# Kernel optimization log

Hardware: AMD Instinct MI355X
Metric: run time of the kernel (lower is better)

The kernel has to match this reference:

```python
import jax, jax.numpy as jnp
import numpy as np

RADIUS = 0.2
NSAMPLE = 32
GROUPS = 4
EPS = 1e-5


def group_norm(x, gamma, beta):
    # x: [B, C, *spatial]; normalize per (batch, group) over channels-in-group + spatial
    B, C = x.shape[0], x.shape[1]
    rest = x.shape[2:]
    xr = x.reshape(B, GROUPS, -1)
    mean = xr.mean(-1, keepdims=True)
    var = xr.var(-1, keepdims=True)
    xr = (xr - mean) * jax.lax.rsqrt(var + EPS)
    x = xr.reshape((B, C) + rest)
    bshape = (1, C) + (1,) * len(rest)
    return x * gamma.reshape(bshape) + beta.reshape(bshape)


def ball_query(pos_t):
    # pos_t: [B, N, 3] -> idx [B, N, NSAMPLE] (query points == all points)
    N = pos_t.shape[1]
    sq = jnp.sum(pos_t * pos_t, axis=-1)  # [B, N]
    d = sq[:, :, None] + sq[:, None, :] - 2.0 * jnp.einsum('bnc,bmc->bnm', pos_t, pos_t)
    ar = jnp.arange(N, dtype=jnp.int32)
    gi = jnp.where(d > RADIUS * RADIUS, N, ar[None, None, :])  # [B, S, N]
    gi = jnp.sort(gi, axis=-1)[:, :, :NSAMPLE]  # ascending in-ball indices first
    first = gi[:, :, :1]
    gi = jnp.where(gi == N, first, gi)  # pad with first neighbor
    return gi


def setup_inputs() -> dict:
    key = jax.random.key(0)
    ks = jax.random.split(key, 6)
    B, C, N = 2, 64, 4096
    M = 4 * C  # mid channels
    return {
        'x': jax.random.normal(ks[0], (B, C, N), jnp.float32),
        'pos': jax.random.uniform(ks[1], (B, 3, N), jnp.float32),
        'w1': jax.random.normal(ks[2], (M, C), jnp.float32) * 0.05,
        'b1': jnp.zeros((M,), jnp.float32),
        'g1': jnp.ones((M,), jnp.float32),
        'be1': jnp.zeros((M,), jnp.float32),
        'wd': 1.0 + jax.random.normal(ks[3], (M,), jnp.float32) * 0.05,
        'gd': jnp.ones((M,), jnp.float32),
        'bed': jnp.zeros((M,), jnp.float32),
        'w2': jax.random.normal(ks[4], (C, M), jnp.float32) * 0.05,
        'b2': jnp.zeros((C,), jnp.float32),
        'g2': jnp.ones((C,), jnp.float32),
        'be2': jnp.zeros((C,), jnp.float32),
    }


def reference(x, pos, w1, b1, g1, be1, wd, gd, bed, w2, b2, g2, be2):
    # x: [B, C, N], pos: [B, 3, N]
    pos_t = jnp.transpose(pos, (0, 2, 1))  # [B, N, 3]
    idx = ball_query(pos_t)  # [B, N, K]

    # conv1 (1x1) -> GroupNorm -> GELU
    h = jnp.einsum('mc,bcn->bmn', w1, x) + b1[None, :, None]
    h = jax.nn.gelu(group_norm(h, g1, be1), approximate=False)  # [B, M, N]

    # gather neighbors: feats [B, N, M] indexed by idx [B, N, K]
    feats = jnp.transpose(h, (0, 2, 1))
    grouped = jax.vmap(lambda f, i: f[i])(feats, idx)  # [B, N, K, M]
    grouped = jnp.transpose(grouped, (0, 3, 1, 2))  # [B, M, N, K]

    # depthwise 1x1 conv (per-channel scale, no bias) -> GroupNorm -> max-pool over K -> GELU
    grouped = grouped * wd[None, :, None, None]
    grouped = group_norm(grouped, gd, bed)
    h2 = jax.nn.gelu(jnp.max(grouped, axis=-1), approximate=False)  # [B, M, N]

    # conv2 (1x1) -> GroupNorm -> residual
    out = jnp.einsum('cm,bmn->bcn', w2, h2) + b2[None, :, None]
    out = group_norm(out, g2, be2)
    return out + x
```

## Files before the change

kernel.cpp:

```cpp
#include <hip/hip_runtime.h>
#include <hip/hip_fp16.h>
#include <math.h>

#define BB 2
#define CC 64
#define NN 4096
#define MM 256
#define KK 32
#define GG 4
#define EPSF 1e-5f

__device__ __forceinline__ float gelu_exact(float x) {
    return 0.5f * x * (1.0f + erff(x * 0.70710678118654752f));
}

__device__ __forceinline__ unsigned pkmax(unsigned a, unsigned b) {
    unsigned d;
    asm volatile("v_pk_max_f16 %0, %1, %2" : "=v"(d) : "v"(a), "v"(b));
    return d;
}
__device__ __forceinline__ unsigned pkmin(unsigned a, unsigned b) {
    unsigned d;
    asm volatile("v_pk_min_f16 %0, %1, %2" : "=v"(d) : "v"(a), "v"(b));
    return d;
// ... 59 lines not shown
        o[1][2] = fmaf(wv.y, xv.z, o[1][2]); o[1][3] = fmaf(wv.y, xv.w, o[1][3]);
        o[2][0] = fmaf(wv.z, xv.x, o[2][0]); o[2][1] = fmaf(wv.z, xv.y, o[2][1]);
        o[2][2] = fmaf(wv.z, xv.z, o[2][2]); o[2][3] = fmaf(wv.z, xv.w, o[2][3]);
        o[3][0] = fmaf(wv.w, xv.x, o[3][0]); o[3][1] = fmaf(wv.w, xv.y, o[3][1]);
        o[3][2] = fmaf(wv.w, xv.z, o[3][2]); o[3][3] = fmaf(wv.w, xv.w, o[3][3]);
    }

    float s1 = 0.f, s2 = 0.f;
    #pragma unroll
    for (int mi = 0; mi < 4; mi++) {
        int m = m0 + mseg * 4 + mi;
        float bv = b1[m];
        float4 r;
        r.x = o[mi][0] + bv; r.y = o[mi][1] + bv;
        r.z = o[mi][2] + bv; r.w = o[mi][3] + bv;
        *(float4*)&h[((size_t)(b * MM + m)) * NN + n0 + nq * 4] = r;
        s1 += r.x + r.y + r.z + r.w;
        s2 = fmaf(r.x, r.x, s2); s2 = fmaf(r.y, r.y, s2);
        s2 = fmaf(r.z, r.z, s2); s2 = fmaf(r.w, r.w, s2);
    }
    for (int off = 32; off; off >>= 1) {
        s1 += __shfl_down(s1, off, 64);
        s2 += __shfl_down(s2, off, 64);
    }
    int w = t >> 6, l = t & 63;
    if (l == 0) { r1[w] = s1; r2[w] = s2; }
    __syncthreads();
    if (t == 0) {
        Mp[bx] = make_float2(r1[0] + r1[1] + r1[2] + r1[3],
                             r2[0] + r2[1] + r2[2] + r2[3]);
    }
}

__global__ void k_gn1t(const float* __restrict__ h, const float* __restrict__ g1,
                       const float* __restrict__ be1, const float* __restrict__ wd,
                       const float2* __restrict__ Mp, __half* __restrict__ pH,
                       float* __restrict__ R) {
    __shared__ float tile[64 * 65];
    __shared__ float mv[2];
    int n0 = blockIdx.x * 64;
    int m0 = blockIdx.y * 64;
    int b  = blockIdx.z;
    int g  = blockIdx.y;
    int t = threadIdx.x;

    if (t < 64) {
        float2 p2 = Mp[b * 256 + g * 64 + t];
        float s1 = p2.x, s2 = p2.y;
        for (int off = 32; off; off >>= 1) {
            s1 += __shfl_down(s1, off, 64);
            s2 += __shfl_down(s2, off, 64);
        }
        if (t == 0) {
            const double cnt = 64.0 * 4096.0;
            double md = (double)s1 / cnt;
            double vd = (double)s2 / cnt - md * md;
            mv[0] = (float)md;
            mv[1] = rsqrtf((float)vd + EPSF);
        }
    }
    __syncthreads();
    float mean = mv[0], rstd = mv[1];

    int nq = t & 15, mr = t >> 4;
    #pragma unroll
    for (int pp = 0; pp < 4; pp++) {
        int row = pp * 16 + mr;
        int m = m0 + row;
        float a = rstd * g1[m];
        float cc2 = be1[m] - mean * a;
        float wdm = wd[m];
        float4 hv = *(const float4*)&h[((size_t)(b * MM + m)) * NN + n0 + nq * 4];
        tile[row * 65 + nq * 4 + 0] = gelu_exact(fmaf(hv.x, a, cc2)) * wdm;
        tile[row * 65 + nq * 4 + 1] = gelu_exact(fmaf(hv.y, a, cc2)) * wdm;
        tile[row * 65 + nq * 4 + 2] = gelu_exact(fmaf(hv.z, a, cc2)) * wdm;
        tile[row * 65 + nq * 4 + 3] = gelu_exact(fmaf(hv.w, a, cc2)) * wdm;
    }
    __syncthreads();
    #pragma unroll
    for (int pp = 0; pp < 4; pp++) {
        int id = pp * 256 + t;
        int nl = id >> 4, mq = id & 15;
        float a0 = tile[(mq * 4 + 0) * 65 + nl];
        float a1 = tile[(mq * 4 + 1) * 65 + nl];
        float a2 = tile[(mq * 4 + 2) * 65 + nl];
        float a3 = tile[(mq * 4 + 3) * 65 + nl];
        __half2 hA = __float22half2_rn(make_float2(a0, a1));
        __half2 hB = __float22half2_rn(make_float2(a2, a3));
        uint2 st8;
        st8.x = *(unsigned*)&hA; st8.y = *(unsigned*)&hB;
        *(uint2*)((char*)pH + ((((size_t)(b * NN) + n0 + nl)) << 9) + (m0 + mq * 4) * 2) = st8;
        float2 fa = __half22float2(hA);
        float2 fb = __half22float2(hB);
        float t1 = fa.x + fa.y + fb.x + fb.y;
        float t2 = fa.x * fa.x + fa.y * fa.y + fb.x * fb.x + fb.y * fb.y;
        #pragma unroll
        for (int off = 8; off; off >>= 1) {
            t1 += __shfl_down(t1, off, 16);
            t2 += __shfl_down(t2, off, 16);
        }
        if ((t & 15) == 0) {
            float* rr = &R[((size_t)(b * NN) + n0 + nl) * 8];
            rr[g]     = t1;
            rr[4 + g] = t2;
        }
    }
}

__global__ void k_ballq(const float* __restrict__ pos, int* __restrict__ idx) {
    int wid  = blockIdx.x * 4 + (threadIdx.x >> 6);
    int lane = threadIdx.x & 63;
    int b = wid >> 12;
    int n = wid & 4095;
    const float* px = pos + b * 3 * NN;
    const float* py = px + NN;
    const float* pz = py + NN;
    float qx = px[n], qy = py[n], qz = pz[n];
    float qsq = qx*qx + qy*qy + qz*qz;
    int* row = idx + (b * NN + n) * KK;

    int found = 0;
    int first = -1;
    const float R2 = 0.04f;
    for (int m0 = 0; m0 < NN && found < KK; m0 += 64) {
        int m = m0 + lane;
        float ax = px[m], ay = py[m], az = pz[m];
        float msq = ax*ax + ay*ay + az*az;
        float dot = qx*ax + qy*ay + qz*az;
        float d = qsq + msq - 2.0f * dot;
        bool hit = !(d > R2);
        unsigned long long mask = __ballot(hit);
        if (first < 0 && mask) first = m0 + (__ffsll((long long)mask) - 1);
        unsigned long long lt = (lane == 0) ? 0ULL : (mask & ((1ULL << lane) - 1ULL));
        int posh = __popcll(lt);
        if (hit && (found + posh) < KK) row[found + posh] = m;
        found += __popcll(mask);
        if (found > KK) found = KK;
    }
    if (lane < KK && lane >= found) row[lane] = first;
}

__global__ __launch_bounds__(256)
void k_qgather(const __half* __restrict__ pH, const int* __restrict__ idx,
               const float* __restrict__ R, const float* __restrict__ gd,
               __half* __restrict__ pselH, float* __restrict__ Rp) {
    int t = threadIdx.x, w = t >> 6, l = t & 63;
    int gn = blockIdx.x * 4 + w;
    int b = gn >> 12;

    int hh = l >> 5, cl = l & 31;
    int myidx = idx[gn * KK + cl];
    const char* pb = (const char*)(pH + (size_t)b * NN * 256);
    int laneoff = cl * 16;

    unsigned vmax0 = 0xFC00FC00u, vmax1 = 0xFC00FC00u, vmax2 = 0xFC00FC00u, vmax3 = 0xFC00FC00u;
    unsigned vmin0 = 0x7C007C00u, vmin1 = 0x7C007C00u, vmin2 = 0x7C007C00u, vmin3 = 0x7C007C00u;

    #pragma unroll
    for (int k = 0; k < 16; k++) {
        int ja = __shfl(myidx, 2 * k, 64);
        int jb = __shfl(myidx, 2 * k + 1, 64);
        int j = hh ? jb : ja;
        uint4 raw = *(const uint4*)(pb + (((size_t)j) << 9) + laneoff);
        vmax0 = pkmax(vmax0, raw.x); vmin0 = pkmin(vmin0, raw.x);
        vmax1 = pkmax(vmax1, raw.y); vmin1 = pkmin(vmin1, raw.y);
        vmax2 = pkmax(vmax2, raw.z); vmin2 = pkmin(vmin2, raw.z);
        vmax3 = pkmax(vmax3, raw.w); vmin3 = pkmin(vmin3, raw.w);
    }
    vmax0 = pkmax(vmax0, (unsigned)__shfl_xor((int)vmax0, 32, 64));
    vmax1 = pkmax(vmax1, (unsigned)__shfl_xor((int)vmax1, 32, 64));
    vmax2 = pkmax(vmax2, (unsigned)__shfl_xor((int)vmax2, 32, 64));
    vmax3 = pkmax(vmax3, (unsigned)__shfl_xor((int)vmax3, 32, 64));
    vmin0 = pkmin(vmin0, (unsigned)__shfl_xor((int)vmin0, 32, 64));
    vmin1 = pkmin(vmin1, (unsigned)__shfl_xor((int)vmin1, 32, 64));
    vmin2 = pkmin(vmin2, (unsigned)__shfl_xor((int)vmin2, 32, 64));
    vmin3 = pkmin(vmin3, (unsigned)__shfl_xor((int)vmin3, 32, 64));

    if (hh == 0) {
        const float4* g4 = (const float4*)gd;
        float4 gA = g4[cl * 2], gB = g4[cl * 2 + 1];
        uint4 out;
        out.x = selpair(vmax0, vmin0, gA.x, gA.y);
        out.y = selpair(vmax1, vmin1, gA.z, gA.w);
        out.z = selpair(vmax2, vmin2, gB.x, gB.y);
        out.w = selpair(vmax3, vmin3, gB.z, gB.w);
        *(uint4*)((char*)pselH + (((size_t)gn) << 9) + laneoff) = out;
    } else {
        const float* rr = &R[((size_t)(b * NN) + myidx) * 8];
        float4 ra = *(const float4*)rr;
        float4 rb = *(const float4*)(rr + 4);
        float s[8] = {ra.x, ra.y, ra.z, ra.w, rb.x, rb.y, rb.z, rb.w};
        #pragma unroll
        for (int off = 16; off; off >>= 1) {
            #pragma unroll
            for (int c = 0; c < 8; c++) s[c] += __shfl_down(s[c], off, 32);
        }
        if (cl == 0) {
            float4* rp = (float4*)&Rp[(size_t)gn * 8];
            rp[0] = make_float4(s[0], s[1], s[2], s[3]);
            rp[1] = make_float4(s[4], s[5], s[6], s[7]);
        }
    }
}

__global__ __launch_bounds__(256, 4)
void k_mlp2(const __half* __restrict__ pselH, const float* __restrict__ Rp,
            const float* __restrict__ w2, const float* __restrict__ b2,
            const float* __restrict__ gd, const float* __restrict__ bed,
            float* __restrict__ oraw, float* __restrict__ Op) {
    __shared__ float w2s[64 * 257];
    __shared__ float sw[4][8];
    __shared__ float sA[4][4], sB[4][4];

    int t = threadIdx.x;
    int w = t >> 6, l = t & 63;
    int b  = blockIdx.x >> 8;
    int n0 = (blockIdx.x & 255) * 16 + w * 4;

    #pragma unroll
    for (int p = 0; p < 16; p++) {
        int i = p * 256 + t;
        int c = i >> 6, mq = i & 63;
        float4 v = ((const float4*)w2)[i];
        float* dst = &w2s[c * 257 + mq * 4];
        dst[0] = v.x; dst[1] = v.y; dst[2] = v.z; dst[3] = v.w;
    }

    {
        const float4* rp = (const float4*)(Rp + (size_t)b * NN * 8);
        float s[8] = {0.f, 0.f, 0.f, 0.f, 0.f, 0.f, 0.f, 0.f};
        #pragma unroll
        for (int r = 0; r < 16; r++) {
            float4 ra = rp[(t * 16 + r) * 2];
            float4 rb = rp[(t * 16 + r) * 2 + 1];
            s[0] += ra.x; s[1] += ra.y; s[2] += ra.z; s[3] += ra.w;
            s[4] += rb.x; s[5] += rb.y; s[6] += rb.z; s[7] += rb.w;
        }
        #pragma unroll
        for (int off = 32; off; off >>= 1) {
            #pragma unroll
            for (int c = 0; c < 8; c++) s[c] += __shfl_down(s[c], off, 64);
        }
        if (l == 0) {
            #pragma unroll
            for (int c = 0; c < 8; c++) sw[w][c] = s[c];
        }
    }
    __syncthreads();

    int g = l >> 4;
    double s1 = (double)sw[0][g] + sw[1][g] + sw[2][g] + sw[3][g];
    double s2 = (double)sw[0][4 + g] + sw[1][4 + g] + sw[2][4 + g] + sw[3][4 + g];
    const double cnt2 = 64.0 * 4096.0 * 32.0;
    double m_ = s1 / cnt2;
    double v_ = s2 / cnt2 - m_ * m_;
    float mean = (float)m_;
    float rstd = rsqrtf((float)v_ + EPSF);
    float4 gd4  = ((const float4*)gd)[l];
    float4 bed4 = ((const float4*)bed)[l];
    float ax = rstd * gd4.x, ay = rstd * gd4.y, az = rstd * gd4.z, aw = rstd * gd4.w;
    float cx = bed4.x - mean * ax, cy = bed4.y - mean * ay;
    float cz = bed4.z - mean * az, cw = bed4.w - mean * aw;

    float4 h2r[4];
    #pragma unroll
    for (int j = 0; j < 4; j++) {
        uint2 raw = *(const uint2*)((const char*)pselH +
                     ((((size_t)(b * NN)) + n0 + j) << 9) + l * 8);
        float2 fa = __half22float2(*(__half2*)&raw.x);
        float2 fb = __half22float2(*(__half2*)&raw.y);
        h2r[j].x = gelu_exact(fmaf(fa.x, ax, cx));
        h2r[j].y = gelu_exact(fmaf(fa.y, ay, cy));
        h2r[j].z = gelu_exact(fmaf(fb.x, az, cz));
        h2r[j].w = gelu_exact(fmaf(fb.y, aw, cw));
    }

    const float* w2l = &w2s[l * 257];
    float acc[4] = {0.f, 0.f, 0.f, 0.f};
    #pragma unroll 8
    for (int mq = 0; mq < 64; mq++) {
        float w0  = w2l[4 * mq + 0];
        float w1_ = w2l[4 * mq + 1];
        float w2_ = w2l[4 * mq + 2];
        float w3_ = w2l[4 * mq + 3];
        #pragma unroll
        for (int j = 0; j < 4; j++) {
            acc[j] = fmaf(w0,  bcast_lane(h2r[j].x, mq), acc[j]);
            acc[j] = fmaf(w1_, bcast_lane(h2r[j].y, mq), acc[j]);
            acc[j] = fmaf(w2_, bcast_lane(h2r[j].z, mq), acc[j]);
            acc[j] = fmaf(w3_, bcast_lane(h2r[j].w, mq), acc[j]);
        }
    }

    float bias = b2[l];
    float so1 = 0.f, so2 = 0.f;
    #pragma unroll
    for (int j = 0; j < 4; j++) {
        acc[j] += bias;
        so1 += acc[j];
        so2 = fmaf(acc[j], acc[j], so2);
    }
    *(float4*)&oraw[((size_t)(b * CC) + l) * NN + n0] =
        make_float4(acc[0], acc[1], acc[2], acc[3]);

    so1 += __shfl_down(so1, 8, 16); so2 += __shfl_down(so2, 8, 16);
    so1 += __shfl_down(so1, 4, 16); so2 += __shfl_down(so2, 4, 16);
    so1 += __shfl_down(so1, 2, 16); so2 += __shfl_down(so2, 2, 16);
    so1 += __shfl_down(so1, 1, 16); so2 += __shfl_down(so2, 1, 16);
    if ((l & 15) == 0) { sA[w][l >> 4] = so1; sB[w][l >> 4] = so2; }
    __syncthreads();
    if (t < 8) {
        int is2 = t >> 2, gg = t & 3;
        float v = is2 ? (sB[0][gg] + sB[1][gg] + sB[2][gg] + sB[3][gg])
                      : (sA[0][gg] + sA[1][gg] + sA[2][gg] + sA[3][gg]);
        Op[blockIdx.x * 8 + t] = v;
    }
}

__global__ void k_final(const float* __restrict__ oraw, const float* __restrict__ x,
                        const float* __restrict__ g2, const float* __restrict__ be2,
                        const float* __restrict__ Op, float* __restrict__ out) {
    __shared__ float fw[4][8];
    int t = threadIdx.x;
    int i4 = blockIdx.x * 256 + t;
    int base = i4 * 4;
    int b = base >> 18;

    {
        const float4* rp = (const float4*)(Op + ((size_t)b * 256 + t) * 8);
        float4 ra = rp[0], rb = rp[1];
        float s[8] = {ra.x, ra.y, ra.z, ra.w, rb.x, rb.y, rb.z, rb.w};
        #pragma unroll
        for (int off = 32; off; off >>= 1) {
            #pragma unroll
            for (int c = 0; c < 8; c++) s[c] += __shfl_down(s[c], off, 64);
        }
        if ((t & 63) == 0) {
            #pragma unroll
            for (int c = 0; c < 8; c++) fw[t >> 6][c] = s[c];
        }
    }
    __syncthreads();

    int c = (base >> 12) & 63;
    int g = c >> 4;
    double s1 = (double)fw[0][g] + fw[1][g] + fw[2][g] + fw[3][g];
    double s2 = (double)fw[0][4 + g] + fw[1][4 + g] + fw[2][4 + g] + fw[3][4 + g];
    const double cnt = 16.0 * 4096.0;
    double mean_d = s1 / cnt;
    double var_d  = s2 / cnt - mean_d * mean_d;
    float mean = (float)mean_d;
    float rstd = rsqrtf((float)var_d + EPSF);
    float sc = rstd * g2[c];
    float ad = be2[c] - mean * sc;
    float4 o = ((const float4*)oraw)[i4];
    float4 xv = ((const float4*)x)[i4];
    float4 r;
    r.x = fmaf(o.x, sc, ad) + xv.x;
    r.y = fmaf(o.y, sc, ad) + xv.y;
    r.z = fmaf(o.z, sc, ad) + xv.z;
    r.w = fmaf(o.w, sc, ad) + xv.w;
    ((float4*)out)[i4] = r;
}

extern "C" void kernel_launch(void* const* d_in, const int* in_sizes, int n_in,
                              void* d_out, int out_size, void* d_ws, size_t ws_size,
                              hipStream_t stream) {
    const float* x   = (const float*)d_in[0];
    const float* pos = (const float*)d_in[1];
    const float* w1  = (const float*)d_in[2];
    const float* b1  = (const float*)d_in[3];
    const float* g1  = (const float*)d_in[4];
    const float* be1 = (const float*)d_in[5];
    const float* wd  = (const float*)d_in[6];
    const float* gd  = (const float*)d_in[7];
    const float* bed = (const float*)d_in[8];
    const float* w2  = (const float*)d_in[9];
    const float* b2  = (const float*)d_in[10];
    const float* g2  = (const float*)d_in[11];
    const float* be2 = (const float*)d_in[12];
    float* out = (float*)d_out;

    char* wsb = (char*)d_ws;
    float*  h     = (float*)wsb;
    __half* pH    = (__half*)(wsb + 8388608);
    __half* pselH = (__half*)(wsb + 12582912);
    float*  oraw  = (float*)(wsb + 16777216);
    int*    idx   = (int*)(wsb + 18874368);
    float*  R     = (float*)(wsb + 19922944);
    float*  Rp    = (float*)(wsb + 20185088);
    float2* Mp    = (float2*)(wsb + 20447232);
    float*  Op    = (float*)(wsb + 20451328);

    k_mlp1<<<512, 256, 0, stream>>>(x, w1, b1, h, Mp);
    k_gn1t<<<dim3(64, 4, 2), 256, 0, stream>>>(h, g1, be1, wd, Mp, pH, R);
    k_ballq<<<2048, 256, 0, stream>>>(pos, idx);
    k_qgather<<<2048, 256, 0, stream>>>(pH, idx, R, gd, pselH, Rp);
    k_mlp2<<<512, 256, 0, stream>>>(pselH, Rp, w2, b2, gd, bed, oraw, Op);
    k_final<<<512, 256, 0, stream>>>(oraw, x, g2, be2, Op, out);
}
```

Baseline: 155.7 us.

## Fuse GN1 with ball query and fold neighbor gather into second MLP

Merges the GroupNorm1/transpose kernel and the ball-query kernel into one launch, with the block index choosing the role. The neighbor gather and max/min pooling move into the second MLP kernel, so the intermediate pooled-feature buffer is no longer written and re-read. A small new kernel computes the grouped GroupNorm statistics from the per-point partial sums. The second MLP kernel now does 32 random gathers per point with 8-byte loads, and its occupancy hint is lowered from 4 to 2 blocks per CU.

Measured after the change: 166.6 us. +7.0%, slower.

```diff
diff --git a/kernel.cpp b/kernel.cpp
--- a/kernel.cpp
+++ b/kernel.cpp
@@ -115,182 +115,162 @@
     }
 }
 
-__global__ void k_gn1t(const float* __restrict__ h, const float* __restrict__ g1,
-                       const float* __restrict__ be1, const float* __restrict__ wd,
-                       const float2* __restrict__ Mp, __half* __restrict__ pH,
-                       float* __restrict__ R) {
+__global__ void k_gn1t_ballq(const float* __restrict__ h, const float* __restrict__ g1,
+                             const float* __restrict__ be1, const float* __restrict__ wd,
+                             const float2* __restrict__ Mp, __half* __restrict__ pH,
+                             float* __restrict__ R,
+                             const float* __restrict__ pos, int* __restrict__ idx) {
     __shared__ float tile[64 * 65];
     __shared__ float mv[2];
-    int n0 = blockIdx.x * 64;
-    int m0 = blockIdx.y * 64;
-    int b  = blockIdx.z;
-    int g  = blockIdx.y;
     int t = threadIdx.x;
 
-    if (t < 64) {
-        float2 p2 = Mp[b * 256 + g * 64 + t];
-        float s1 = p2.x, s2 = p2.y;
-        for (int off = 32; off; off >>= 1) {
-            s1 += __shfl_down(s1, off, 64);
-            s2 += __shfl_down(s2, off, 64);
-        }
-        if (t == 0) {
-            const double cnt = 64.0 * 4096.0;
-            double md = (double)s1 / cnt;
-            double vd = (double)s2 / cnt - md * md;
-            mv[0] = (float)md;
-            mv[1] = rsqrtf((float)vd + EPSF);
-        }
-    }
-    __syncthreads();
-    float mean = mv[0], rstd = mv[1];
-
-    int nq = t & 15, mr = t >> 4;
-    #pragma unroll
-    for (int pp = 0; pp < 4; pp++) {
-        int row = pp * 16 + mr;
-        int m = m0 + row;
-        float a = rstd * g1[m];
-        float cc2 = be1[m] - mean * a;
-        float wdm = wd[m];
-        float4 hv = *(const float4*)&h[((size_t)(b * MM + m)) * NN + n0 + nq * 4];
-        tile[row * 65 + nq * 4 + 0] = gelu_exact(fmaf(hv.x, a, cc2)) * wdm;
-        tile[row * 65 + nq * 4 + 1] = gelu_exact(fmaf(hv.y, a, cc2)) * wdm;
-        tile[row * 65 + nq * 4 + 2] = gelu_exact(fmaf(hv.z, a, cc2)) * wdm;
-        tile[row * 65 + nq * 4 + 3] = gelu_exact(fmaf(hv.w, a, cc2)) * wdm;
-    }
-    __syncthreads();
-    #pragma unroll
-    for (int pp = 0; pp < 4; pp++) {
-        int id = pp * 256 + t;
-        int nl = id >> 4, mq = id & 15;
-        float a0 = tile[(mq * 4 + 0) * 65 + nl];
-        float a1 = tile[(mq * 4 + 1) * 65 + nl];
-        float a2 = tile[(mq * 4 + 2) * 65 + nl];
-        float a3 = tile[(mq * 4 + 3) * 65 + nl];
-        __half2 hA = __float22half2_rn(make_float2(a0, a1));
-        __half2 hB = __float22half2_rn(make_float2(a2, a3));
-        uint2 st8;
-        st8.x = *(unsigned*)&hA; st8.y = *(unsigned*)&hB;
-        *(uint2*)((char*)pH + ((((size_t)(b * NN) + n0 + nl)) << 9) + (m0 + mq * 4) * 2) = st8;
-        float2 fa = __half22float2(hA);
-        float2 fb = __half22float2(hB);
-        float t1 = fa.x + fa.y + fb.x + fb.y;
-        float t2 = fa.x * fa.x + fa.y * fa.y + fb.x * fb.x + fb.y * fb.y;
-        #pragma unroll
-        for (int off = 8; off; off >>= 1) {
-            t1 += __shfl_down(t1, off, 16);
-            t2 += __shfl_down(t2, off, 16);
-        }
-        if ((t & 15) == 0) {
-            float* rr = &R[((size_t)(b * NN) + n0 + nl) * 8];
-            rr[g]     = t1;
-            rr[4 + g] = t2;
-        }
-    }
-}
-
-__global__ void k_ballq(const float* __restrict__ pos, int* __restrict__ idx) {
-    int wid  = blockIdx.x * 4 + (threadIdx.x >> 6);
-    int lane = threadIdx.x & 63;
-    int b = wid >> 12;
-    int n = wid & 4095;
-    const float* px = pos + b * 3 * NN;
-    const float* py = px + NN;
-    const float* pz = py + NN;
-    float qx = px[n], qy = py[n], qz = pz[n];
-    float qsq = qx*qx + qy*qy + qz*qz;
-    int* row = idx + (b * NN + n) * KK;
-
-    int found = 0;
-    int first = -1;
-    const float R2 = 0.04f;
-    for (int m0 = 0; m0 < NN && found < KK; m0 += 64) {
-        int m = m0 + lane;
-        float ax = px[m], ay = py[m], az = pz[m];
-        float msq = ax*ax + ay*ay + az*az;
-        float dot = qx*ax + qy*ay + qz*az;
-        float d = qsq + msq - 2.0f * dot;
-        bool hit = !(d > R2);
-        unsigned long long mask = __ballot(hit);
-        if (first < 0 && mask) first = m0 + (__ffsll((long long)mask) - 1);
-        unsigned long long lt = (lane == 0) ? 0ULL : (mask & ((1ULL << lane) - 1ULL));
-        int posh = __popcll(lt);
-        if (hit && (found + posh) < KK) row[found + posh] = m;
-        found += __popcll(mask);
-        if (found > KK) found = KK;
-    }
-    if (lane < KK && lane >= found) row[lane] = first;
-}
-
-__global__ __launch_bounds__(256)
-void k_qgather(const __half* __restrict__ pH, const int* __restrict__ idx,
-               const float* __restrict__ R, const float* __restrict__ gd,
-               __half* __restrict__ pselH, float* __restrict__ Rp) {
-    int t = threadIdx.x, w = t >> 6, l = t & 63;
-    int gn = blockIdx.x * 4 + w;
-    int b = gn >> 12;
-
-    int hh = l >> 5, cl = l & 31;
-    int myidx = idx[gn * KK + cl];
-    const char* pb = (const char*)(pH + (size_t)b * NN * 256);
-    int laneoff = cl * 16;
-
-    unsigned vmax0 = 0xFC00FC00u, vmax1 = 0xFC00FC00u, vmax2 = 0xFC00FC00u, vmax3 = 0xFC00FC00u;
-    unsigned vmin0 = 0x7C007C00u, vmin1 = 0x7C007C00u, vmin2 = 0x7C007C00u, vmin3 = 0x7C007C00u;
-
-    #pragma unroll
-    for (int k = 0; k < 16; k++) {
-        int ja = __shfl(myidx, 2 * k, 64);
-        int jb = __shfl(myidx, 2 * k + 1, 64);
-        int j = hh ? jb : ja;
-        uint4 raw = *(const uint4*)(pb + (((size_t)j) << 9) + laneoff);
-        vmax0 = pkmax(vmax0, raw.x); vmin0 = pkmin(vmin0, raw.x);
-        vmax1 = pkmax(vmax1, raw.y); vmin1 = pkmin(vmin1, raw.y);
-        vmax2 = pkmax(vmax2, raw.z); vmin2 = pkmin(vmin2, raw.z);
-        vmax3 = pkmax(vmax3, raw.w); vmin3 = pkmin(vmin3, raw.w);
-    }
-    vmax0 = pkmax(vmax0, (unsigned)__shfl_xor((int)vmax0, 32, 64));
-    vmax1 = pkmax(vmax1, (unsigned)__shfl_xor((int)vmax1, 32, 64));
-    vmax2 = pkmax(vmax2, (unsigned)__shfl_xor((int)vmax2, 32, 64));
-    vmax3 = pkmax(vmax3, (unsigned)__shfl_xor((int)vmax3, 32, 64));
-    vmin0 = pkmin(vmin0, (unsigned)__shfl_xor((int)vmin0, 32, 64));
-    vmin1 = pkmin(vmin1, (unsigned)__shfl_xor((int)vmin1, 32, 64));
-    vmin2 = pkmin(vmin2, (unsigned)__shfl_xor((int)vmin2, 32, 64));
-    vmin3 = pkmin(vmin3, (unsigned)__shfl_xor((int)vmin3, 32, 64));
-
-    if (hh == 0) {
-        const float4* g4 = (const float4*)gd;
-        float4 gA = g4[cl * 2], gB = g4[cl * 2 + 1];
-        uint4 out;
-        out.x = selpair(vmax0, vmin0, gA.x, gA.y);
-        out.y = selpair(vmax1, vmin1, gA.z, gA.w);
-        out.z = selpair(vmax2, vmin2, gB.x, gB.y);
-        out.w = selpair(vmax3, vmin3, gB.z, gB.w);
-        *(uint4*)((char*)pselH + (((size_t)gn) << 9) + laneoff) = out;
+    if (blockIdx.x < 512) {
+        int id = blockIdx.x;
+        int n0 = (id & 63) * 64;
+        int g  = (id >> 6) & 3;
+        int b  = id >> 8;
+        int m0 = g * 64;
+
+        if (t < 64) {
+            float2 p2 = Mp[b * 256 + g * 64 + t];
+            float s1 = p2.x, s2 = p2.y;
+            for (int off = 32; off; off >>= 1) {
+                s1 += __shfl_down(s1, off, 64);
+                s2 += __shfl_down(s2, off, 64);
+            }
+            if (t == 0) {
+                const double cnt = 64.0 * 4096.0;
+                double md = (double)s1 / cnt;
+                double vd = (double)s2 / cnt - md * md;
+                mv[0] = (float)md;
+                mv[1] = rsqrtf((float)vd + EPSF);
+            }
+        }
+        __syncthreads();
+        float mean = mv[0], rstd = mv[1];
+
+        int nq = t & 15, mr = t >> 4;
+        #pragma unroll
+        for (int pp = 0; pp < 4; pp++) {
+            int row = pp * 16 + mr;
+            int m = m0 + row;
+            float a = rstd * g1[m];
+            float cc2 = be1[m] - mean * a;
+            float wdm = wd[m];
+            float4 hv = *(const float4*)&h[((size_t)(b * MM + m)) * NN + n0 + nq * 4];
+            tile[row * 65 + nq * 4 + 0] = gelu_exact(fmaf(hv.x, a, cc2)) * wdm;
+            tile[row * 65 + nq * 4 + 1] = gelu_exact(fmaf(hv.y, a, cc2)) * wdm;
+            tile[row * 65 + nq * 4 + 2] = gelu_exact(fmaf(hv.z, a, cc2)) * wdm;
+            tile[row * 65 + nq * 4 + 3] = gelu_exact(fmaf(hv.w, a, cc2)) * wdm;
+        }
+        __syncthreads();
+        #pragma unroll
+        for (int pp = 0; pp < 4; pp++) {
+            int id2 = pp * 256 + t;
+            int nl = id2 >> 4, mq = id2 & 15;
+            float a0 = tile[(mq * 4 + 0) * 65 + nl];
+            float a1 = tile[(mq * 4 + 1) * 65 + nl];
+            float a2 = tile[(mq * 4 + 2) * 65 + nl];
+            float a3 = tile[(mq * 4 + 3) * 65 + nl];
+            __half2 hA = __float22half2_rn(make_float2(a0, a1));
+            __half2 hB = __float22half2_rn(make_float2(a2, a3));
+            uint2 st8;
+            st8.x = *(unsigned*)&hA; st8.y = *(unsigned*)&hB;
+            *(uint2*)((char*)pH + ((((size_t)(b * NN) + n0 + nl)) << 9) + (m0 + mq * 4) * 2) = st8;
+            float2 fa = __half22float2(hA);
+            float2 fb = __half22float2(hB);
+            float t1 = fa.x + fa.y + fb.x + fb.y;
+            float t2 = fa.x * fa.x + fa.y * fa.y + fb.x * fb.x + fb.y * fb.y;
+            #pragma unroll
+            for (int off = 8; off; off >>= 1) {
+                t1 += __shfl_down(t1, off, 16);
+                t2 += __shfl_down(t2, off, 16);
+            }
+            if ((t & 15) == 0) {
+                float* rr = &R[((size_t)(b * NN) + n0 + nl) * 8];
+                rr[g]     = t1;
+                rr[4 + g] = t2;
+            }
+        }
     } else {
-        const float* rr = &R[((size_t)(b * NN) + myidx) * 8];
+        int bx = blockIdx.x - 512;
+        int wid  = bx * 4 + (threadIdx.x >> 6);
+        int lane = threadIdx.x & 63;
+        int b = wid >> 12;
+        int n = wid & 4095;
+        const float* px = pos + b * 3 * NN;
+        const float* py = px + NN;
+        const float* pz = py + NN;
+        float qx = px[n], qy = py[n], qz = pz[n];
+        float qsq = qx*qx + qy*qy + qz*qz;
+        int* row = idx + (b * NN + n) * KK;
+
+        int found = 0;
+        int first = -1;
+        const float R2 = 0.04f;
+        for (int m0 = 0; m0 < NN && found < KK; m0 += 64) {
+            int m = m0 + lane;
+            float ax = px[m], ay = py[m], az = pz[m];
+            float msq = ax*ax + ay*ay + az*az;
+            float dot = qx*ax + qy*ay + qz*az;
+            float d = qsq + msq - 2.0f * dot;
+            bool hit = !(d > R2);
+            unsigned long long mask = __ballot(hit);
+            if (first < 0 && mask) first = m0 + (__ffsll((long long)mask) - 1);
+            unsigned long long lt = (lane == 0) ? 0ULL : (mask & ((1ULL << lane) - 1ULL));
+            int posh = __popcll(lt);
+            if (hit && (found + posh) < KK) row[found + posh] = m;
+            found += __popcll(mask);
+            if (found > KK) found = KK;
+        }
+        if (lane < KK && lane >= found) row[lane] = first;
+    }
+}
+
+__global__ void k_gstats(const int* __restrict__ idx, const float* __restrict__ R,
+                         float* __restrict__ Gp) {
+    __shared__ float sAcc[8][8];
+    int t = threadIdx.x;
+    int hw = t >> 5, cl = t & 31;
+    int pbase = blockIdx.x * 32;
+    int b = pbase >> 12;
+    float s[8];
+    #pragma unroll
+    for (int c = 0; c < 8; c++) s[c] = 0.f;
+    #pragma unroll
+    for (int it = 0; it < 4; it++) {
+        int pt = pbase + it * 8 + hw;
+        int j = idx[pt * KK + cl];
+        const float* rr = &R[((size_t)(b * NN) + j) * 8];
         float4 ra = *(const float4*)rr;
         float4 rb = *(const float4*)(rr + 4);
-        float s[8] = {ra.x, ra.y, ra.z, ra.w, rb.x, rb.y, rb.z, rb.w};
-        #pragma unroll
-        for (int off = 16; off; off >>= 1) {
-            #pragma unroll
-            for (int c = 0; c < 8; c++) s[c] += __shfl_down(s[c], off, 32);
-        }
-        if (cl == 0) {
-            float4* rp = (float4*)&Rp[(size_t)gn * 8];
-            rp[0] = make_float4(s[0], s[1], s[2], s[3]);
-            rp[1] = make_float4(s[4], s[5], s[6], s[7]);
-        }
-    }
-}
-
-__global__ __launch_bounds__(256, 4)
-void k_mlp2(const __half* __restrict__ pselH, const float* __restrict__ Rp,
-            const float* __restrict__ w2, const float* __restrict__ b2,
-            const float* __restrict__ gd, const float* __restrict__ bed,
-            float* __restrict__ oraw, float* __restrict__ Op) {
+        s[0] += ra.x; s[1] += ra.y; s[2] += ra.z; s[3] += ra.w;
+        s[4] += rb.x; s[5] += rb.y; s[6] += rb.z; s[7] += rb.w;
+    }
+    #pragma unroll
+    for (int off = 16; off; off >>= 1) {
+        #pragma unroll
+        for (int c = 0; c < 8; c++) s[c] += __shfl_down(s[c], off, 32);
+    }
+    if (cl == 0) {
+        #pragma unroll
+        for (int c = 0; c < 8; c++) sAcc[hw][c] = s[c];
+    }
+    __syncthreads();
+    if (t < 8) {
+        float v = 0.f;
+        #pragma unroll
+        for (int k = 0; k < 8; k++) v += sAcc[k][t];
+        Gp[blockIdx.x * 8 + t] = v;
+    }
+}
+
+__global__ __launch_bounds__(256, 2)
+void k_gmlp2(const __half* __restrict__ pH, const int* __restrict__ idx,
+             const float* __restrict__ Gp,
+             const float* __restrict__ w2, const float* __restrict__ b2,
+             const float* __restrict__ gd, const float* __restrict__ bed,
+             float* __restrict__ oraw, float* __restrict__ Op) {
     __shared__ float w2s[64 * 257];
     __shared__ float sw[4][8];
     __shared__ float sA[4][4], sB[4][4];
@@ -310,14 +290,12 @@
     }
 
     {
-        const float4* rp = (const float4*)(Rp + (size_t)b * NN * 8);
         float s[8] = {0.f, 0.f, 0.f, 0.f, 0.f, 0.f, 0.f, 0.f};
-        #pragma unroll
-        for (int r = 0; r < 16; r++) {
-            float4 ra = rp[(t * 16 + r) * 2];
-            float4 rb = rp[(t * 16 + r) * 2 + 1];
-            s[0] += ra.x; s[1] += ra.y; s[2] += ra.z; s[3] += ra.w;
-            s[4] += rb.x; s[5] += rb.y; s[6] += rb.z; s[7] += rb.w;
+        if (t < 128) {
+            const float4* gp = (const float4*)(Gp + ((size_t)(b * 128 + t)) * 8);
+            float4 ra = gp[0], rb = gp[1];
+            s[0] = ra.x; s[1] = ra.y; s[2] = ra.z; s[3] = ra.w;
+            s[4] = rb.x; s[5] = rb.y; s[6] = rb.z; s[7] = rb.w;
         }
         #pragma unroll
         for (int off = 32; off; off >>= 1) {
@@ -329,6 +307,29 @@
             for (int c = 0; c < 8; c++) sw[w][c] = s[c];
         }
     }
+
+    int regH0 = idx[((size_t)(b * NN) + n0 + (l >> 5)) * KK + (l & 31)];
+    int regH1 = idx[((size_t)(b * NN) + n0 + 2 + (l >> 5)) * KK + (l & 31)];
+
+    const char* pb = (const char*)(pH + (size_t)b * NN * 256);
+    unsigned vmx[4][2], vmn[4][2];
+    #pragma unroll
+    for (int jj = 0; jj < 4; jj++) {
+        vmx[jj][0] = 0xFC00FC00u; vmx[jj][1] = 0xFC00FC00u;
+        vmn[jj][0] = 0x7C007C00u; vmn[jj][1] = 0x7C007C00u;
+    }
+    #pragma unroll
+    for (int jj = 0; jj < 4; jj++) {
+        int rh = (jj < 2) ? regH0 : regH1;
+        #pragma unroll 8
+        for (int k = 0; k < 32; k++) {
+            int j = __shfl(rh, ((jj & 1) << 5) + k, 64);
+            uint2 raw = *(const uint2*)(pb + (((size_t)j) << 9) + l * 8);
+            vmx[jj][0] = pkmax(vmx[jj][0], raw.x); vmn[jj][0] = pkmin(vmn[jj][0], raw.x);
+            vmx[jj][1] = pkmax(vmx[jj][1], raw.y); vmn[jj][1] = pkmin(vmn[jj][1], raw.y);
+        }
+    }
+
     __syncthreads();
 
     int g = l >> 4;
@@ -347,15 +348,15 @@
 
     float4 h2r[4];
     #pragma unroll
-    for (int j = 0; j < 4; j++) {
-        uint2 raw = *(const uint2*)((const char*)pselH +
-                     ((((size_t)(b * NN)) + n0 + j) << 9) + l * 8);
-        float2 fa = __half22float2(*(__half2*)&raw.x);
-        float2 fb = __half22float2(*(__half2*)&raw.y);
-        h2r[j].x = gelu_exact(fmaf(fa.x, ax, cx));
-        h2r[j].y = gelu_exact(fmaf(fa.y, ay, cy));
-        h2r[j].z = gelu_exact(fmaf(fb.x, az, cz));
-        h2r[j].w = gelu_exact(fmaf(fb.y, aw, cw));
+    for (int jj = 0; jj < 4; jj++) {
+        unsigned sel0 = selpair(vmx[jj][0], vmn[jj][0], gd4.x, gd4.y);
+        unsigned sel1 = selpair(vmx[jj][1], vmn[jj][1], gd4.z, gd4.w);
+        float2 fa = __half22float2(*(__half2*)&sel0);
+        float2 fb = __half22float2(*(__half2*)&sel1);
+        h2r[jj].x = gelu_exact(fmaf(fa.x, ax, cx));
+        h2r[jj].y = gelu_exact(fmaf(fa.y, ay, cy));
+        h2r[jj].z = gelu_exact(fmaf(fb.x, az, cz));
+        h2r[jj].w = gelu_exact(fmaf(fb.y, aw, cw));
     }
 
     const float* w2l = &w2s[l * 257];
@@ -467,18 +468,16 @@
     char* wsb = (char*)d_ws;
     float*  h     = (float*)wsb;
     __half* pH    = (__half*)(wsb + 8388608);
-    __half* pselH = (__half*)(wsb + 12582912);
-    float*  oraw  = (float*)(wsb + 16777216);
-    int*    idx   = (int*)(wsb + 18874368);
-    float*  R     = (float*)(wsb + 19922944);
-    float*  Rp    = (float*)(wsb + 20185088);
-    float2* Mp    = (float2*)(wsb + 20447232);
-    float*  Op    = (float*)(wsb + 20451328);
+    float*  oraw  = (float*)(wsb + 12582912);
+    int*    idx   = (int*)(wsb + 14680064);
+    float*  R     = (float*)(wsb + 15728640);
+    float2* Mp    = (float2*)(wsb + 15990784);
+    float*  Gp    = (float*)(wsb + 15994880);
+    float*  Op    = (float*)(wsb + 16003072);
 
     k_mlp1<<<512, 256, 0, stream>>>(x, w1, b1, h, Mp);
-    k_gn1t<<<dim3(64, 4, 2), 256, 0, stream>>>(h, g1, be1, wd, Mp, pH, R);
-    k_ballq<<<2048, 256, 0, stream>>>(pos, idx);
-    k_qgather<<<2048, 256, 0, stream>>>(pH, idx, R, gd, pselH, Rp);
-    k_mlp2<<<512, 256, 0, stream>>>(pselH, Rp, w2, b2, gd, bed, oraw, Op);
+    k_gn1t_ballq<<<2560, 256, 0, stream>>>(h, g1, be1, wd, Mp, pH, R, pos, idx);
+    k_gstats<<<256, 256, 0, stream>>>(idx, R, Gp);
+    k_gmlp2<<<512, 256, 0, stream>>>(pH, idx, Gp, w2, b2, gd, bed, oraw, Op);
     k_final<<<512, 256, 0, stream>>>(oraw, x, g2, be2, Op, out);
 }
```

## Merge GN1 with ball query, restructure gather stats, widen mlp2 tiles

Applied to the files above, without the earlier changes.

Independent kernels k_gn1t and k_ballq are merged into one launch using block-index ranges, which cuts a launch and lets the two jobs overlap. The qgather kernel's per-point group-stat lanes become separate blocks that pre-reduce stats into a compact Gp buffer, so mlp2 no longer sums 4096 per-point partials. mlp2 now processes 8 points per wave with half as many blocks, which raises register pressure and lowers parallelism.

Measured after the change: 148.9 us. -4.4%, faster.

```diff
diff --git a/kernel.cpp b/kernel.cpp
--- a/kernel.cpp
+++ b/kernel.cpp
@@ -115,179 +115,207 @@
     }
 }
 
-__global__ void k_gn1t(const float* __restrict__ h, const float* __restrict__ g1,
-                       const float* __restrict__ be1, const float* __restrict__ wd,
-                       const float2* __restrict__ Mp, __half* __restrict__ pH,
-                       float* __restrict__ R) {
+__global__ void k_gn1t_ballq(const float* __restrict__ h, const float* __restrict__ g1,
+                             const float* __restrict__ be1, const float* __restrict__ wd,
+                             const float2* __restrict__ Mp, __half* __restrict__ pH,
+                             float* __restrict__ R,
+                             const float* __restrict__ pos, int* __restrict__ idx) {
     __shared__ float tile[64 * 65];
     __shared__ float mv[2];
-    int n0 = blockIdx.x * 64;
-    int m0 = blockIdx.y * 64;
-    int b  = blockIdx.z;
-    int g  = blockIdx.y;
     int t = threadIdx.x;
 
-    if (t < 64) {
-        float2 p2 = Mp[b * 256 + g * 64 + t];
-        float s1 = p2.x, s2 = p2.y;
-        for (int off = 32; off; off >>= 1) {
-            s1 += __shfl_down(s1, off, 64);
-            s2 += __shfl_down(s2, off, 64);
-        }
-        if (t == 0) {
-            const double cnt = 64.0 * 4096.0;
-            double md = (double)s1 / cnt;
-            double vd = (double)s2 / cnt - md * md;
-            mv[0] = (float)md;
-            mv[1] = rsqrtf((float)vd + EPSF);
-        }
-    }
-    __syncthreads();
-    float mean = mv[0], rstd = mv[1];
-
-    int nq = t & 15, mr = t >> 4;
-    #pragma unroll
-    for (int pp = 0; pp < 4; pp++) {
-        int row = pp * 16 + mr;
-        int m = m0 + row;
-        float a = rstd * g1[m];
-        float cc2 = be1[m] - mean * a;
-        float wdm = wd[m];
-        float4 hv = *(const float4*)&h[((size_t)(b * MM + m)) * NN + n0 + nq * 4];
-        tile[row * 65 + nq * 4 + 0] = gelu_exact(fmaf(hv.x, a, cc2)) * wdm;
-        tile[row * 65 + nq * 4 + 1] = gelu_exact(fmaf(hv.y, a, cc2)) * wdm;
-        tile[row * 65 + nq * 4 + 2] = gelu_exact(fmaf(hv.z, a, cc2)) * wdm;
-        tile[row * 65 + nq * 4 + 3] = gelu_exact(fmaf(hv.w, a, cc2)) * wdm;
-    }
-    __syncthreads();
-    #pragma unroll
-    for (int pp = 0; pp < 4; pp++) {
-        int id = pp * 256 + t;
-        int nl = id >> 4, mq = id & 15;
-        float a0 = tile[(mq * 4 + 0) * 65 + nl];
-        float a1 = tile[(mq * 4 + 1) * 65 + nl];
-        float a2 = tile[(mq * 4 + 2) * 65 + nl];
-        float a3 = tile[(mq * 4 + 3) * 65 + nl];
-        __half2 hA = __float22half2_rn(make_float2(a0, a1));
-        __half2 hB = __float22half2_rn(make_float2(a2, a3));
-        uint2 st8;
-        st8.x = *(unsigned*)&hA; st8.y = *(unsigned*)&hB;
-        *(uint2*)((char*)pH + ((((size_t)(b * NN) + n0 + nl)) << 9) + (m0 + mq * 4) * 2) = st8;
-        float2 fa = __half22float2(hA);
-        float2 fb = __half22float2(hB);
-        float t1 = fa.x + fa.y + fb.x + fb.y;
-        float t2 = fa.x * fa.x + fa.y * fa.y + fb.x * fb.x + fb.y * fb.y;
-        #pragma unroll
-        for (int off = 8; off; off >>= 1) {
-            t1 += __shfl_down(t1, off, 16);
-            t2 += __shfl_down(t2, off, 16);
-        }
-        if ((t & 15) == 0) {
-            float* rr = &R[((size_t)(b * NN) + n0 + nl) * 8];
-            rr[g]     = t1;
-            rr[4 + g] = t2;
-        }
-    }
-}
-
-__global__ void k_ballq(const float* __restrict__ pos, int* __restrict__ idx) {
-    int wid  = blockIdx.x * 4 + (threadIdx.x >> 6);
-    int lane = threadIdx.x & 63;
-    int b = wid >> 12;
-    int n = wid & 4095;
-    const float* px = pos + b * 3 * NN;
-    const float* py = px + NN;
-    const float* pz = py + NN;
-    float qx = px[n], qy = py[n], qz = pz[n];
-    float qsq = qx*qx + qy*qy + qz*qz;
-    int* row = idx + (b * NN + n) * KK;
-
-    int found = 0;
-    int first = -1;
-    const float R2 = 0.04f;
-    for (int m0 = 0; m0 < NN && found < KK; m0 += 64) {
-        int m = m0 + lane;
-        float ax = px[m], ay = py[m], az = pz[m];
-        float msq = ax*ax + ay*ay + az*az;
-        float dot = qx*ax + qy*ay + qz*az;
-        float d = qsq + msq - 2.0f * dot;
-        bool hit = !(d > R2);
-        unsigned long long mask = __ballot(hit);
-        if (first < 0 && mask) first = m0 + (__ffsll((long long)mask) - 1);
-        unsigned long long lt = (lane == 0) ? 0ULL : (mask & ((1ULL << lane) - 1ULL));
-        int posh = __popcll(lt);
-        if (hit && (found + posh) < KK) row[found + posh] = m;
-        found += __popcll(mask);
-        if (found > KK) found = KK;
-    }
-    if (lane < KK && lane >= found) row[lane] = first;
+    if (blockIdx.x < 512) {
+        int id = blockIdx.x;
+        int n0 = (id & 63) * 64;
+        int g  = (id >> 6) & 3;
+        int b  = id >> 8;
+        int m0 = g * 64;
+
+        if (t < 64) {
+            float2 p2 = Mp[b * 256 + g * 64 + t];
+            float s1 = p2.x, s2 = p2.y;
+            for (int off = 32; off; off >>= 1) {
+                s1 += __shfl_down(s1, off, 64);
+                s2 += __shfl_down(s2, off, 64);
+            }
+            if (t == 0) {
+                const double cnt = 64.0 * 4096.0;
+                double md = (double)s1 / cnt;
+                double vd = (double)s2 / cnt - md * md;
+                mv[0] = (float)md;
+                mv[1] = rsqrtf((float)vd + EPSF);
+            }
+        }
+        __syncthreads();
+        float mean = mv[0], rstd = mv[1];
+
+        int nq = t & 15, mr = t >> 4;
+        #pragma unroll
+        for (int pp = 0; pp < 4; pp++) {
+            int row = pp * 16 + mr;
+            int m = m0 + row;
+            float a = rstd * g1[m];
+            float cc2 = be1[m] - mean * a;
+            float wdm = wd[m];
+            float4 hv = *(const float4*)&h[((size_t)(b * MM + m)) * NN + n0 + nq * 4];
+            tile[row * 65 + nq * 4 + 0] = gelu_exact(fmaf(hv.x, a, cc2)) * wdm;
+            tile[row * 65 + nq * 4 + 1] = gelu_exact(fmaf(hv.y, a, cc2)) * wdm;
+            tile[row * 65 + nq * 4 + 2] = gelu_exact(fmaf(hv.z, a, cc2)) * wdm;
+            tile[row * 65 + nq * 4 + 3] = gelu_exact(fmaf(hv.w, a, cc2)) * wdm;
+        }
+        __syncthreads();
+        #pragma unroll
+        for (int pp = 0; pp < 4; pp++) {
+            int id2 = pp * 256 + t;
+            int nl = id2 >> 4, mq = id2 & 15;
+            float a0 = tile[(mq * 4 + 0) * 65 + nl];
+            float a1 = tile[(mq * 4 + 1) * 65 + nl];
+            float a2 = tile[(mq * 4 + 2) * 65 + nl];
+            float a3 = tile[(mq * 4 + 3) * 65 + nl];
+            __half2 hA = __float22half2_rn(make_float2(a0, a1));
+            __half2 hB = __float22half2_rn(make_float2(a2, a3));
+            uint2 st8;
+            st8.x = *(unsigned*)&hA; st8.y = *(unsigned*)&hB;
+            *(uint2*)((char*)pH + ((((size_t)(b * NN) + n0 + nl)) << 9) + (m0 + mq * 4) * 2) = st8;
+            float2 fa = __half22float2(hA);
+            float2 fb = __half22float2(hB);
+            float t1 = fa.x + fa.y + fb.x + fb.y;
+            float t2 = fa.x * fa.x + fa.y * fa.y + fb.x * fb.x + fb.y * fb.y;
+            #pragma unroll
+            for (int off = 8; off; off >>= 1) {
+                t1 += __shfl_down(t1, off, 16);
+                t2 += __shfl_down(t2, off, 16);
+            }
+            if ((t & 15) == 0) {
+                float* rr = &R[((size_t)(b * NN) + n0 + nl) * 8];
+                rr[g]     = t1;
+                rr[4 + g] = t2;
+            }
+        }
+    } else {
+        int bx = blockIdx.x - 512;
+        int wid  = bx * 4 + (threadIdx.x >> 6);
+        int lane = threadIdx.x & 63;
+        int b = wid >> 12;
+        int n = wid & 4095;
+        const float* px = pos + b * 3 * NN;
+        const float* py = px + NN;
+        const float* pz = py + NN;
+        float qx = px[n], qy = py[n], qz = pz[n];
+        float qsq = qx*qx + qy*qy + qz*qz;
+        int* row = idx + (b * NN + n) * KK;
+
+        int found = 0;
+        int first = -1;
+        const float R2 = 0.04f;
+        for (int m0 = 0; m0 < NN && found < KK; m0 += 64) {
+            int m = m0 + lane;
+            float ax = px[m], ay = py[m], az = pz[m];
+            float msq = ax*ax + ay*ay + az*az;
+            float dot = qx*ax + qy*ay + qz*az;
+            float d = qsq + msq - 2.0f * dot;
+            bool hit = !(d > R2);
+            unsigned long long mask = __ballot(hit);
+            if (first < 0 && mask) first = m0 + (__ffsll((long long)mask) - 1);
+            unsigned long long lt = (lane == 0) ? 0ULL : (mask & ((1ULL << lane) - 1ULL));
+            int posh = __popcll(lt);
+            if (hit && (found + posh) < KK) row[found + posh] = m;
+            found += __popcll(mask);
+            if (found > KK) found = KK;
+        }
+        if (lane < KK && lane >= found) row[lane] = first;
+    }
 }
 
 __global__ __launch_bounds__(256)
-void k_qgather(const __half* __restrict__ pH, const int* __restrict__ idx,
-               const float* __restrict__ R, const float* __restrict__ gd,
-               __half* __restrict__ pselH, float* __restrict__ Rp) {
-    int t = threadIdx.x, w = t >> 6, l = t & 63;
-    int gn = blockIdx.x * 4 + w;
-    int b = gn >> 12;
-
-    int hh = l >> 5, cl = l & 31;
-    int myidx = idx[gn * KK + cl];
-    const char* pb = (const char*)(pH + (size_t)b * NN * 256);
-    int laneoff = cl * 16;
-
-    unsigned vmax0 = 0xFC00FC00u, vmax1 = 0xFC00FC00u, vmax2 = 0xFC00FC00u, vmax3 = 0xFC00FC00u;
-    unsigned vmin0 = 0x7C007C00u, vmin1 = 0x7C007C00u, vmin2 = 0x7C007C00u, vmin3 = 0x7C007C00u;
-
-    #pragma unroll
-    for (int k = 0; k < 16; k++) {
-        int ja = __shfl(myidx, 2 * k, 64);
-        int jb = __shfl(myidx, 2 * k + 1, 64);
-        int j = hh ? jb : ja;
-        uint4 raw = *(const uint4*)(pb + (((size_t)j) << 9) + laneoff);
-        vmax0 = pkmax(vmax0, raw.x); vmin0 = pkmin(vmin0, raw.x);
-        vmax1 = pkmax(vmax1, raw.y); vmin1 = pkmin(vmin1, raw.y);
-        vmax2 = pkmax(vmax2, raw.z); vmin2 = pkmin(vmin2, raw.z);
-        vmax3 = pkmax(vmax3, raw.w); vmin3 = pkmin(vmin3, raw.w);
-    }
-    vmax0 = pkmax(vmax0, (unsigned)__shfl_xor((int)vmax0, 32, 64));
-    vmax1 = pkmax(vmax1, (unsigned)__shfl_xor((int)vmax1, 32, 64));
-    vmax2 = pkmax(vmax2, (unsigned)__shfl_xor((int)vmax2, 32, 64));
-    vmax3 = pkmax(vmax3, (unsigned)__shfl_xor((int)vmax3, 32, 64));
-    vmin0 = pkmin(vmin0, (unsigned)__shfl_xor((int)vmin0, 32, 64));
-    vmin1 = pkmin(vmin1, (unsigned)__shfl_xor((int)vmin1, 32, 64));
-    vmin2 = pkmin(vmin2, (unsigned)__shfl_xor((int)vmin2, 32, 64));
-    vmin3 = pkmin(vmin3, (unsigned)__shfl_xor((int)vmin3, 32, 64));
-
-    if (hh == 0) {
-        const float4* g4 = (const float4*)gd;
-        float4 gA = g4[cl * 2], gB = g4[cl * 2 + 1];
-        uint4 out;
-        out.x = selpair(vmax0, vmin0, gA.x, gA.y);
-        out.y = selpair(vmax1, vmin1, gA.z, gA.w);
-        out.z = selpair(vmax2, vmin2, gB.x, gB.y);
-        out.w = selpair(vmax3, vmin3, gB.z, gB.w);
-        *(uint4*)((char*)pselH + (((size_t)gn) << 9) + laneoff) = out;
+void k_qgather_gstats(const __half* __restrict__ pH, const int* __restrict__ idx,
+                      const float* __restrict__ R, const float* __restrict__ gd,
+                      __half* __restrict__ pselH, float* __restrict__ Gp) {
+    __shared__ float sAcc[8][8];
+    int t = threadIdx.x;
+
+    if (blockIdx.x < 2048) {
+        int w = t >> 6, l = t & 63;
+        int gn = blockIdx.x * 4 + w;
+        int b = gn >> 12;
+
+        int hh = l >> 5, cl = l & 31;
+        int myidx = idx[gn * KK + cl];
+        const char* pb = (const char*)(pH + (size_t)b * NN * 256);
+        int laneoff = cl * 16;
+
+        unsigned vmax0 = 0xFC00FC00u, vmax1 = 0xFC00FC00u, vmax2 = 0xFC00FC00u, vmax3 = 0xFC00FC00u;
+        unsigned vmin0 = 0x7C007C00u, vmin1 = 0x7C007C00u, vmin2 = 0x7C007C00u, vmin3 = 0x7C007C00u;
+
+        #pragma unroll
+        for (int k = 0; k < 16; k++) {
+            int ja = __shfl(myidx, 2 * k, 64);
+            int jb = __shfl(myidx, 2 * k + 1, 64);
+            int j = hh ? jb : ja;
+            uint4 raw = *(const uint4*)(pb + (((size_t)j) << 9) + laneoff);
+            vmax0 = pkmax(vmax0, raw.x); vmin0 = pkmin(vmin0, raw.x);
+            vmax1 = pkmax(vmax1, raw.y); vmin1 = pkmin(vmin1, raw.y);
+            vmax2 = pkmax(vmax2, raw.z); vmin2 = pkmin(vmin2, raw.z);
+            vmax3 = pkmax(vmax3, raw.w); vmin3 = pkmin(vmin3, raw.w);
+        }
+        vmax0 = pkmax(vmax0, (unsigned)__shfl_xor((int)vmax0, 32, 64));
+        vmax1 = pkmax(vmax1, (unsigned)__shfl_xor((int)vmax1, 32, 64));
+        vmax2 = pkmax(vmax2, (unsigned)__shfl_xor((int)vmax2, 32, 64));
+        vmax3 = pkmax(vmax3, (unsigned)__shfl_xor((int)vmax3, 32, 64));
+        vmin0 = pkmin(vmin0, (unsigned)__shfl_xor((int)vmin0, 32, 64));
+        vmin1 = pkmin(vmin1, (unsigned)__shfl_xor((int)vmin1, 32, 64));
+        vmin2 = pkmin(vmin2, (unsigned)__shfl_xor((int)vmin2, 32, 64));
+        vmin3 = pkmin(vmin3, (unsigned)__shfl_xor((int)vmin3, 32, 64));
+
+        if (hh == 0) {
+            const float4* g4 = (const float4*)gd;
+            float4 gA = g4[cl * 2], gB = g4[cl * 2 + 1];
+            uint4 out;
+            out.x = selpair(vmax0, vmin0, gA.x, gA.y);
+            out.y = selpair(vmax1, vmin1, gA.z, gA.w);
+            out.z = selpair(vmax2, vmin2, gB.x, gB.y);
+            out.w = selpair(vmax3, vmin3, gB.z, gB.w);
+            *(uint4*)((char*)pselH + (((size_t)gn) << 9) + laneoff) = out;
+        }
     } else {
-        const float* rr = &R[((size_t)(b * NN) + myidx) * 8];
-        float4 ra = *(const float4*)rr;
-        float4 rb = *(const float4*)(rr + 4);
-        float s[8] = {ra.x, ra.y, ra.z, ra.w, rb.x, rb.y, rb.z, rb.w};
+        int bid = blockIdx.x - 2048;
+        int hw = t >> 5, cl = t & 31;
+        int pbase = bid * 32;
+        int b = pbase >> 12;
+        float s[8];
+        #pragma unroll
+        for (int c = 0; c < 8; c++) s[c] = 0.f;
+        #pragma unroll
+        for (int it = 0; it < 4; it++) {
+            int pt = pbase + it * 8 + hw;
+            int j = idx[pt * KK + cl];
+            const float* rr = &R[((size_t)(b * NN) + j) * 8];
+            float4 ra = *(const float4*)rr;
+            float4 rb = *(const float4*)(rr + 4);
+            s[0] += ra.x; s[1] += ra.y; s[2] += ra.z; s[3] += ra.w;
+            s[4] += rb.x; s[5] += rb.y; s[6] += rb.z; s[7] += rb.w;
+        }
         #pragma unroll
         for (int off = 16; off; off >>= 1) {
             #pragma unroll
             for (int c = 0; c < 8; c++) s[c] += __shfl_down(s[c], off, 32);
         }
         if (cl == 0) {
-            float4* rp = (float4*)&Rp[(size_t)gn * 8];
-            rp[0] = make_float4(s[0], s[1], s[2], s[3]);
-            rp[1] = make_float4(s[4], s[5], s[6], s[7]);
+            #pragma unroll
+            for (int c = 0; c < 8; c++) sAcc[hw][c] = s[c];
+        }
+        __syncthreads();
+        if (t < 8) {
+            float v = 0.f;
+            #pragma unroll
+            for (int k = 0; k < 8; k++) v += sAcc[k][t];
+            Gp[bid * 8 + t] = v;
         }
     }
 }
 
 __global__ __launch_bounds__(256, 4)
-void k_mlp2(const __half* __restrict__ pselH, const float* __restrict__ Rp,
+void k_mlp2(const __half* __restrict__ pselH, const float* __restrict__ Gp,
             const float* __restrict__ w2, const float* __restrict__ b2,
             const float* __restrict__ gd, const float* __restrict__ bed,
             float* __restrict__ oraw, float* __restrict__ Op) {
@@ -297,8 +325,8 @@
 
     int t = threadIdx.x;
     int w = t >> 6, l = t & 63;
-    int b  = blockIdx.x >> 8;
-    int n0 = (blockIdx.x & 255) * 16 + w * 4;
+    int b  = blockIdx.x >> 7;
+    int n0 = (blockIdx.x & 127) * 32 + w * 8;
 
     #pragma unroll
     for (int p = 0; p < 16; p++) {
@@ -310,14 +338,12 @@
     }
 
     {
-        const float4* rp = (const float4*)(Rp + (size_t)b * NN * 8);
         float s[8] = {0.f, 0.f, 0.f, 0.f, 0.f, 0.f, 0.f, 0.f};
-        #pragma unroll
-        for (int r = 0; r < 16; r++) {
-            float4 ra = rp[(t * 16 + r) * 2];
-            float4 rb = rp[(t * 16 + r) * 2 + 1];
-            s[0] += ra.x; s[1] += ra.y; s[2] += ra.z; s[3] += ra.w;
-            s[4] += rb.x; s[5] += rb.y; s[6] += rb.z; s[7] += rb.w;
+        if (t < 128) {
+            const float4* gp = (const float4*)(Gp + ((size_t)(b * 128 + t)) * 8);
+            float4 ra = gp[0], rb = gp[1];
+            s[0] = ra.x; s[1] = ra.y; s[2] = ra.z; s[3] = ra.w;
+            s[4] = rb.x; s[5] = rb.y; s[6] = rb.z; s[7] = rb.w;
         }
         #pragma unroll
         for (int off = 32; off; off >>= 1) {
@@ -345,9 +371,9 @@
     float cx = bed4.x - mean * ax, cy = bed4.y - mean * ay;
     float cz = bed4.z - mean * az, cw = bed4.w - mean * aw;
 
-    float4 h2r[4];
+    float4 h2r[8];
     #pragma unroll
-    for (int j = 0; j < 4; j++) {
+    for (int j = 0; j < 8; j++) {
         uint2 raw = *(const uint2*)((const char*)pselH +
                      ((((size_t)(b * NN)) + n0 + j) << 9) + l * 8);
         float2 fa = __half22float2(*(__half2*)&raw.x);
@@ -359,7 +385,10 @@
     }
 
     const float* w2l = &w2s[l * 257];
-    float acc[4] = {0.f, 0.f, 0.f, 0.f};
+    float acc[8];
+    #pragma unroll
+    for (int j = 0; j < 8; j++) acc[j] = 0.f;
+
     #pragma unroll 8
     for (int mq = 0; mq < 64; mq++) {
         float w0  = w2l[4 * mq + 0];
@@ -367,7 +396,7 @@
         float w2_ = w2l[4 * mq + 2];
         float w3_ = w2l[4 * mq + 3];
         #pragma unroll
-        for (int j = 0; j < 4; j++) {
+        for (int j = 0; j < 8; j++) {
             acc[j] = fmaf(w0,  bcast_lane(h2r[j].x, mq), acc[j]);
             acc[j] = fmaf(w1_, bcast_lane(h2r[j].y, mq), acc[j]);
             acc[j] = fmaf(w2_, bcast_lane(h2r[j].z, mq), acc[j]);
@@ -378,13 +407,14 @@
     float bias = b2[l];
     float so1 = 0.f, so2 = 0.f;
     #pragma unroll
-    for (int j = 0; j < 4; j++) {
+    for (int j = 0; j < 8; j++) {
         acc[j] += bias;
         so1 += acc[j];
         so2 = fmaf(acc[j], acc[j], so2);
     }
-    *(float4*)&oraw[((size_t)(b * CC) + l) * NN + n0] =
-        make_float4(acc[0], acc[1], acc[2], acc[3]);
+    float* dst = &oraw[((size_t)(b * CC) + l) * NN + n0];
+    *(float4*)&dst[0] = make_float4(acc[0], acc[1], acc[2], acc[3]);
+    *(float4*)&dst[4] = make_float4(acc[4], acc[5], acc[6], acc[7]);
 
     so1 += __shfl_down(so1, 8, 16); so2 += __shfl_down(so2, 8, 16);
     so1 += __shfl_down(so1, 4, 16); so2 += __shfl_down(so2, 4, 16);
@@ -410,9 +440,13 @@
     int b = base >> 18;
 
     {
-        const float4* rp = (const float4*)(Op + ((size_t)b * 256 + t) * 8);
-        float4 ra = rp[0], rb = rp[1];
-        float s[8] = {ra.x, ra.y, ra.z, ra.w, rb.x, rb.y, rb.z, rb.w};
+        float s[8] = {0.f, 0.f, 0.f, 0.f, 0.f, 0.f, 0.f, 0.f};
+        if (t < 128) {
+            const float4* rp = (const float4*)(Op + ((size_t)(b * 128 + t)) * 8);
+            float4 ra = rp[0], rb = rp[1];
+            s[0] = ra.x; s[1] = ra.y; s[2] = ra.z; s[3] = ra.w;
+            s[4] = rb.x; s[5] = rb.y; s[6] = rb.z; s[7] = rb.w;
+        }
         #pragma unroll
         for (int off = 32; off; off >>= 1) {
             #pragma unroll
@@ -471,14 +505,13 @@
     float*  oraw  = (float*)(wsb + 16777216);
     int*    idx   = (int*)(wsb + 18874368);
     float*  R     = (float*)(wsb + 19922944);
-    float*  Rp    = (float*)(wsb + 20185088);
-    float2* Mp    = (float2*)(wsb + 20447232);
-    float*  Op    = (float*)(wsb + 20451328);
+    float2* Mp    = (float2*)(wsb + 20185088);
+    float*  Gp    = (float*)(wsb + 20189184);
+    float*  Op    = (float*)(wsb + 20197376);
 
     k_mlp1<<<512, 256, 0, stream>>>(x, w1, b1, h, Mp);
-    k_gn1t<<<dim3(64, 4, 2), 256, 0, stream>>>(h, g1, be1, wd, Mp, pH, R);
-    k_ballq<<<2048, 256, 0, stream>>>(pos, idx);
-    k_qgather<<<2048, 256, 0, stream>>>(pH, idx, R, gd, pselH, Rp);
-    k_mlp2<<<512, 256, 0, stream>>>(pselH, Rp, w2, b2, gd, bed, oraw, Op);
+    k_gn1t_ballq<<<2560, 256, 0, stream>>>(h, g1, be1, wd, Mp, pH, R, pos, idx);
+    k_qgather_gstats<<<2304, 256, 0, stream>>>(pH, idx, R, gd, pselH, Gp);
+    k_mlp2<<<256, 256, 0, stream>>>(pselH, Gp, w2, b2, gd, bed, oraw, Op);
     k_final<<<512, 256, 0, stream>>>(oraw, x, g2, be2, Op, out);
 }
```
